# Performance work log

Hardware: AMD Instinct MI355X
Metric: run time of the kernel (lower is better)

The kernel has to match this reference:

```python
import jax, jax.numpy as jnp
import numpy as np

N_NODES = 100000
N_EDGES = 1600000
D_IN = 13      # per-localization feature dim
D_POS = 3
HIDDEN = 64
D_OUT = 64


def setup_inputs() -> dict:
    key = jax.random.key(0)
    ks = jax.random.split(key, 6)
    x_locs = jax.random.normal(ks[0], (N_NODES, D_IN), dtype=jnp.float32)
    pos_locs = jax.random.uniform(ks[1], (N_NODES, D_POS), dtype=jnp.float32)
    edge_index = jax.random.randint(ks[2], (2, N_EDGES), 0, N_NODES, dtype=jnp.int64)
    fan1 = D_IN + D_POS
    W1 = jax.random.normal(ks[3], (fan1, HIDDEN), dtype=jnp.float32) / np.sqrt(fan1)
    b1 = jnp.zeros((HIDDEN,), dtype=jnp.float32)
    W2 = jax.random.normal(ks[4], (HIDDEN, D_OUT), dtype=jnp.float32) / np.sqrt(HIDDEN)
    b2 = jnp.zeros((D_OUT,), dtype=jnp.float32)
    return {"x_locs": x_locs, "pos_locs": pos_locs, "W1": W1, "b1": b1,
            "W2": W2, "b2": b2, "edge_index": edge_index}


def reference(x_locs, pos_locs, W1, b1, W2, b2, edge_index):
    # PointNetConv (source_to_target): j = edge_index[0] (source), i = edge_index[1] (target)
    src = edge_index[0]
    dst = edge_index[1]
    # message input: [x_j, pos_j - pos_i]  -> [E, D_IN + D_POS]
    msg_in = jnp.concatenate([x_locs[src], pos_locs[src] - pos_locs[dst]], axis=-1)
    # local_nn: Linear -> ReLU -> Linear
    h = jax.nn.relu(msg_in @ W1 + b1)            # [E, HIDDEN]
    h = h @ W2 + b2                               # [E, D_OUT]
    # max aggregation per target node; empty segments get -inf
    agg = jax.ops.segment_max(h, dst, num_segments=N_NODES)  # [N, D_OUT]
    # final .relu() in LocEncoder; also maps empty (-inf) segments to 0 (PyG convention)
    return jax.nn.relu(agg)
```

## Files before the change

kernel.cpp:

```cpp
#include <hip/hip_runtime.h>
#include <hip/hip_bf16.h>


#define N_NODES 100000
#define N_EDGES 1600000
#define NB2  782
#define NBLK 391
#define BATCH 4096
#define SCAP 2400

typedef short short8  __attribute__((ext_vector_type(8)));
typedef float float4v __attribute__((ext_vector_type(4)));

__device__ inline short f2bf(float f) {
    union { float f; unsigned u; } v; v.f = f;
    unsigned u = v.u;
    u += 0x7fffu + ((u >> 16) & 1u);
    return (short)(u >> 16);
}
__device__ inline short2 f2bf2(float a, float b) {
    __hip_bfloat162 h = __float22bfloat162_rn(make_float2(a, b));
    return *(short2*)&h;
}
__device__ inline float bf2f(short s) {
    union { unsigned u; float f; } v;
    v.u = ((unsigned)(unsigned short)s) << 16;
    return v.f;
}
__device__ inline int wave_incl_scan(int v, int lane) {
#pragma unroll
    for (int d = 1; d < 64; d <<= 1) {
        const int t = __shfl_up(v, d);
        if (lane >= d) v += t;
    }
    return v;
}

__global__ __launch_bounds__(256) void prep_kernel(
    const float* __restrict__ x, const float* __restrict__ pos,
    const float* __restrict__ W1, const float* __restrict__ b1,
    const int* __restrict__ ei,
    int* __restrict__ offsT,
    int* __restrict__ blockSorted,
    unsigned short* __restrict__ u16, unsigned short* __restrict__ w16)
{
    __shared__ int hist[NB2], eoff[NB2], offc[NB2];
    __shared__ int csumP[13];

    const int tid  = threadIdx.x;
    const int lane = tid & 63;
    const int wv   = tid >> 6;

    if (blockIdx.x >= NBLK) {
        float w1c[16];
#pragma unroll
        for (int k = 0; k < 16; ++k) w1c[k] = W1[k * 64 + lane];
        const float b1c = b1[lane];

        const int waveId = (blockIdx.x - NBLK) * 4 + wv;
        const int nwave  = 512 * 4;

        for (int node = waveId; node < N_NODES; node += nwave) {
            float m = 0.f;
            if (lane < 13) m = x[node * 13 + lane];
            else if (lane < 16) m = pos[node * 3 + (lane - 13)];

            float acc = b1c, accw = 0.f;
#pragma unroll
            for (int k = 0; k < 13; ++k)
                acc = fmaf(__shfl(m, k), w1c[k], acc);
#pragma unroll
            for (int k = 13; k < 16; ++k) {
                const float p = __shfl(m, k);
                acc  = fmaf(p, w1c[k], acc);
                accw = fmaf(p, w1c[k], accw);
            }
            u16[node * 64 + lane] = (unsigned short)f2bf(acc);
            w16[node * 64 + lane] = (unsigned short)f2bf(accw);
        }
        return;
    }

    const int blk = blockIdx.x;
    const int e0  = blk * BATCH;
    const int nn  = (N_EDGES - e0) < BATCH ? (N_EDGES - e0) : BATCH;

    for (int i = tid; i < NB2; i += 256) hist[i] = 0;
    __syncthreads();

#pragma unroll
    for (int rep = 0; rep < 4; ++rep) {
        const int base = rep * 1024 + tid * 4;
        if (base < nn) {
            const int4 d4 = *(const int4*)(ei + N_EDGES + e0 + base);
            atomicAdd(&hist[d4.x >> 7], 1);
            atomicAdd(&hist[d4.y >> 7], 1);
            atomicAdd(&hist[d4.z >> 7], 1);
            atomicAdd(&hist[d4.w >> 7], 1);
        }
    }
    __syncthreads();

    for (int c = wv; c < 13; c += 4) {
        const int idx = c * 64 + lane;
        const int val = (idx < NB2) ? hist[idx] : 0;
        const int inc = wave_incl_scan(val, lane);
        if (idx < NB2) eoff[idx] = inc;
        if (lane == 63) csumP[c] = inc;
    }
    __syncthreads();
    if (tid == 0) {
        int a = 0;
#pragma unroll
        for (int c = 0; c < 13; ++c) { const int t = csumP[c]; csumP[c] = a; a += t; }
    }
    __syncthreads();
    for (int c = wv; c < 13; c += 4) {
        const int idx = c * 64 + lane;
        if (idx < NB2) eoff[idx] += csumP[c] - hist[idx];
    }
    __syncthreads();

    for (int b = tid; b < NB2; b += 256) {
        offsT[b * NBLK + blk] = eoff[b];
        offc[b] = eoff[b];
    }
    if (tid == 0) offsT[NB2 * NBLK + blk] = nn;
    __syncthreads();

    int* dstp = blockSorted + blk * BATCH;
#pragma unroll
    for (int rep = 0; rep < 4; ++rep) {
        const int base = rep * 1024 + tid * 4;
        if (base < nn) {
            const int4 s4 = *(const int4*)(ei + e0 + base);
            const int4 d4 = *(const int4*)(ei + N_EDGES + e0 + base);
            int p;
            p = atomicAdd(&offc[d4.x >> 7], 1); dstp[p] = (s4.x << 7) | (d4.x & 127);
            p = atomicAdd(&offc[d4.y >> 7], 1); dstp[p] = (s4.y << 7) | (d4.y & 127);
            p = atomicAdd(&offc[d4.z >> 7], 1); dstp[p] = (s4.z << 7) | (d4.z & 127);
            p = atomicAdd(&offc[d4.w >> 7], 1); dstp[p] = (s4.w << 7) | (d4.w & 127);
        }
    }
}

__global__ __launch_bounds__(256, 4) void aggregate_kernel(
    const unsigned short* __restrict__ u16,
    const unsigned short* __restrict__ w16,
    const float* __restrict__ W2,
    const float* __restrict__ b2,
    const int*   __restrict__ offsT,
    const int*   __restrict__ blockSorted,
    float*       __restrict__ out)
{
    __shared__ int staged[SCAP];
    __shared__ int sortedL[SCAP];
    __shared__ int E[NBLK], G[NBLK];
    __shared__ int hist[128], hoff[128], nstart[128];
    __shared__ int csum[8];
    __shared__ int totT;

    const int tid  = threadIdx.x;
    const int lane = tid & 63;
    const int wv   = tid >> 6;
    const int q = lane >> 4, n = lane & 15;
    const int b = blockIdx.x;
    const int node0 = b * 128;

    short8 w2f[2][4];
#pragma unroll
    for (int s = 0; s < 2; ++s)
#pragma unroll
        for (int t = 0; t < 4; ++t)
#pragma unroll
            for (int j = 0; j < 8; ++j)
                w2f[s][t][j] = f2bf(W2[(s * 32 + q * 8 + j) * 64 + (n + 16 * t)]);
    float b2c[4];
#pragma unroll
    for (int t = 0; t < 4; ++t) b2c[t] = b2[n + 16 * t];

    if (tid < 128) hist[tid] = 0;

    for (int r = tid; r < NBLK; r += 256) {
        const int lo = offsT[b * NBLK + r];
        const int hi = offsT[(b + 1) * NBLK + r];
        staged[r] = hi - lo;
        G[r] = r * BATCH + lo;
    }
    __syncthreads();
    for (int c = wv; c < 7; c += 4) {
        const int idx = c * 64 + lane;
        const int val = (idx < NBLK) ? staged[idx] : 0;
        const int inc = wave_incl_scan(val, lane);
        if (idx < NBLK) E[idx] = inc;
        if (lane == 63) csum[c] = inc;
    }
    __syncthreads();
    if (tid == 0) {
        int a = 0;
#pragma unroll
        for (int c = 0; c < 7; ++c) { const int t = csum[c]; csum[c] = a; a += t; }
        totT = a;
    }
    __syncthreads();
    for (int c = wv; c < 7; c += 4) {
        const int idx = c * 64 + lane;
        if (idx < NBLK) E[idx] += csum[c] - staged[idx];
    }
    __syncthreads();

    int T = totT; T = T < SCAP ? T : SCAP;

    for (int i = tid; i < T; i += 256) {
        int lo = 0, hi = NBLK - 1;
#pragma unroll
        for (int s = 0; s < 9; ++s) {
            const int mid = (lo + hi + 1) >> 1;
            if (E[mid] <= i) lo = mid; else hi = mid - 1;
        }
        const int w = blockSorted[G[lo] + (i - E[lo])];
        staged[i] = w;
        atomicAdd(&hist[w & 127], 1);
    }
    __syncthreads();

    if (wv < 2) {
        const int v = hist[tid];
        const int inc = wave_incl_scan(v, lane);
        nstart[tid] = inc - v;
        if (lane == 63) csum[wv] = inc;
    }
    __syncthreads();
    if (tid >= 64 && tid < 128) nstart[tid] += csum[0];
    __syncthreads();
    if (tid < 128) hoff[tid] = nstart[tid];
    __syncthreads();
    for (int i = tid; i < T; i += 256) {
        const int w = staged[i];
        const int p = atomicAdd(&hoff[w & 127], 1);
        sortedL[p] = w >> 7;
    }
    __syncthreads();

    auto compute = [&](int node, int2 sd, int src,
                       short8 ulo, short8 uhi, short8 wl, short8 wh) {
        float vmax[4] = {0.f, 0.f, 0.f, 0.f};
        int base = 0;
        while (true) {
            const int rows = (sd.y - base) < 16 ? (sd.y - base) : 16;
            if (rows > 0) {
                union { short8 v; short2 h[4]; } alo, ahi;
#pragma unroll
                for (int j = 0; j < 4; ++j) {
                    alo.h[j] = f2bf2(
                        fmaxf(bf2f(ulo[2*j])   - bf2f(wl[2*j]),   0.f),
                        fmaxf(bf2f(ulo[2*j+1]) - bf2f(wl[2*j+1]), 0.f));
                    ahi.h[j] = f2bf2(
                        fmaxf(bf2f(uhi[2*j])   - bf2f(wh[2*j]),   0.f),
                        fmaxf(bf2f(uhi[2*j+1]) - bf2f(wh[2*j+1]), 0.f));
                }
                float4v c2[4];
#pragma unroll
                for (int t = 0; t < 4; ++t) {
                    c2[t] = __builtin_amdgcn_mfma_f32_16x16x32_bf16(
                        alo.v, w2f[0][t], (float4v){0.f, 0.f, 0.f, 0.f}, 0, 0, 0);
                    c2[t] = __builtin_amdgcn_mfma_f32_16x16x32_bf16(
                        ahi.v, w2f[1][t], c2[t], 0, 0, 0);
                }
#pragma unroll
                for (int r = 0; r < 4; ++r) {
                    const int row = q * 4 + r;
#pragma unroll
                    for (int t = 0; t < 4; ++t) {
                        const float v = c2[t][r] + b2c[t];
                        if (row < rows) vmax[t] = fmaxf(vmax[t], v);
                    }
                }
            }
            base += 16;
            if (base >= sd.y) break;
            const int r2 = (sd.y - base) < 16 ? (sd.y - base) : 16;
            src = (n < r2) ? sortedL[sd.x + base + n] : 0;
            ulo = *(const short8*)(u16 + src * 64 + q * 8);
            uhi = *(const short8*)(u16 + src * 64 + 32 + q * 8);
        }
#pragma unroll
        for (int t = 0; t < 4; ++t) {
            vmax[t] = fmaxf(vmax[t], __shfl_xor(vmax[t], 16));
            vmax[t] = fmaxf(vmax[t], __shfl_xor(vmax[t], 32));
        }
        float v = vmax[0];
        v = (q == 1) ? vmax[1] : v;
        v = (q == 2) ? vmax[2] : v;
        v = (q == 3) ? vmax[3] : v;
        if (node < N_NODES) out[node * 64 + lane] = v;
    };

    const int nlbase = wv * 32;
#pragma unroll 1
    for (int g = 0; g < 32; g += 2) {
        const int nlA = nlbase + g, nlB = nlA + 1;
        const int nA = node0 + nlA, nB = node0 + nlB;
        const int2 sdA = {nstart[nlA], hist[nlA]};
        const int2 sdB = {nstart[nlB], hist[nlB]};
        const int nAc = nA < (N_NODES - 1) ? nA : (N_NODES - 1);
        const int nBc = nB < (N_NODES - 1) ? nB : (N_NODES - 1);

        const int rA = sdA.y < 16 ? sdA.y : 16;
        const int rB = sdB.y < 16 ? sdB.y : 16;
        const int srcA = (n < rA) ? sortedL[sdA.x + n] : 0;
        const int srcB = (n < rB) ? sortedL[sdB.x + n] : 0;

        const short8 ulA = *(const short8*)(u16 + srcA * 64 + q * 8);
        const short8 uhA = *(const short8*)(u16 + srcA * 64 + 32 + q * 8);
        const short8 wlA = *(const short8*)(w16 + nAc * 64 + q * 8);
        const short8 whA = *(const short8*)(w16 + nAc * 64 + 32 + q * 8);
        const short8 ulB = *(const short8*)(u16 + srcB * 64 + q * 8);
        const short8 uhB = *(const short8*)(u16 + srcB * 64 + 32 + q * 8);
        const short8 wlB = *(const short8*)(w16 + nBc * 64 + q * 8);
        const short8 whB = *(const short8*)(w16 + nBc * 64 + 32 + q * 8);

        compute(nA, sdA, srcA, ulA, uhA, wlA, whA);
        compute(nB, sdB, srcB, ulB, uhB, wlB, whB);
    }
}

extern "C" void kernel_launch(void* const* d_in, const int* in_sizes, int n_in,
                              void* d_out, int out_size, void* d_ws, size_t ws_size,
                              hipStream_t stream) {
    const float* x   = (const float*)d_in[0];
    const float* pos = (const float*)d_in[1];
    const float* W1  = (const float*)d_in[2];
    const float* b1  = (const float*)d_in[3];
    const float* W2  = (const float*)d_in[4];
    const float* b2  = (const float*)d_in[5];
    const int*   ei  = (const int*)d_in[6];

    char* ws = (char*)d_ws;
    int* blockSorted = (int*)(ws + 0);
    int* offsT       = (int*)(ws + 6406144);
    unsigned short* u16 = (unsigned short*)(ws + 7631360);
    unsigned short* w16 = (unsigned short*)(ws + 20431360);

    prep_kernel<<<NBLK + 512, 256, 0, stream>>>(
        x, pos, W1, b1, ei, offsT, blockSorted, u16, w16);
    aggregate_kernel<<<NB2, 256, 0, stream>>>(
        u16, w16, W2, b2, offsT, blockSorted, (float*)d_out);
}
```

Before: 213.1 us.

## Switch to fp16 packed math, 64-node buckets, and split prep into two kernels

Replaces the bf16 storage and the manual bf16 convert/relu with fp16 values, so the relu-subtract runs as packed half vector ops and the MFMA uses the f16 variant. Halves the bucket width from 128 to 64 nodes, so the aggregate launches twice as many blocks with smaller shared staging. Splits the fused prep kernel into separate precompute and partition kernels, and the precompute now handles two nodes per wave iteration. This removes per-element conversion ALU work and increases parallelism, at the cost of an extra launch, fp16 range risk, and more offset scanning per aggregate block.

```diff
diff --git a/kernel.cpp b/kernel.cpp
--- a/kernel.cpp
+++ b/kernel.cpp
@@ -1,32 +1,16 @@
 #include <hip/hip_runtime.h>
-#include <hip/hip_bf16.h>
 
 
 #define N_NODES 100000
 #define N_EDGES 1600000
-#define NB2  782
+#define NB2  1563
 #define NBLK 391
 #define BATCH 4096
-#define SCAP 2400
-
-typedef short short8  __attribute__((ext_vector_type(8)));
+#define SCAP2 1280
+
+typedef _Float16 half8 __attribute__((ext_vector_type(8)));
 typedef float float4v __attribute__((ext_vector_type(4)));
 
-__device__ inline short f2bf(float f) {
-    union { float f; unsigned u; } v; v.f = f;
-    unsigned u = v.u;
-    u += 0x7fffu + ((u >> 16) & 1u);
-    return (short)(u >> 16);
-}
-__device__ inline short2 f2bf2(float a, float b) {
-    __hip_bfloat162 h = __float22bfloat162_rn(make_float2(a, b));
-    return *(short2*)&h;
-}
-__device__ inline float bf2f(short s) {
-    union { unsigned u; float f; } v;
-    v.u = ((unsigned)(unsigned short)s) << 16;
-    return v.f;
-}
 __device__ inline int wave_incl_scan(int v, int lane) {
 #pragma unroll
     for (int d = 1; d < 64; d <<= 1) {
@@ -36,54 +20,64 @@
     return v;
 }
 
-__global__ __launch_bounds__(256) void prep_kernel(
+__global__ __launch_bounds__(256) void precompute_kernel(
     const float* __restrict__ x, const float* __restrict__ pos,
     const float* __restrict__ W1, const float* __restrict__ b1,
+    _Float16* __restrict__ u16, _Float16* __restrict__ w16)
+{
+    const int lane = threadIdx.x & 63;
+    float w1c[16];
+#pragma unroll
+    for (int k = 0; k < 16; ++k) w1c[k] = W1[k * 64 + lane];
+    const float b1c = b1[lane];
+
+    const int waveId = blockIdx.x * 4 + (threadIdx.x >> 6);
+    const int step   = 512 * 4 * 2;
+
+    for (int nd = waveId * 2; nd < N_NODES; nd += step) {
+        const int nA = nd, nB = nd + 1;
+        float mA = 0.f, mB = 0.f;
+        if (lane < 13) {
+            mA = x[nA * 13 + lane];
+            mB = x[nB * 13 + lane];
+        } else if (lane < 16) {
+            mA = pos[nA * 3 + (lane - 13)];
+            mB = pos[nB * 3 + (lane - 13)];
+        }
+
+        float aA = b1c, wA = 0.f, aB = b1c, wB = 0.f;
+#pragma unroll
+        for (int k = 0; k < 13; ++k) {
+            aA = fmaf(__shfl(mA, k), w1c[k], aA);
+            aB = fmaf(__shfl(mB, k), w1c[k], aB);
+        }
+#pragma unroll
+        for (int k = 13; k < 16; ++k) {
+            const float pA = __shfl(mA, k), pB = __shfl(mB, k);
+            aA = fmaf(pA, w1c[k], aA);  wA = fmaf(pA, w1c[k], wA);
+            aB = fmaf(pB, w1c[k], aB);  wB = fmaf(pB, w1c[k], wB);
+        }
+        u16[nA * 64 + lane] = (_Float16)aA;
+        w16[nA * 64 + lane] = (_Float16)wA;
+        u16[nB * 64 + lane] = (_Float16)aB;
+        w16[nB * 64 + lane] = (_Float16)wB;
+    }
+}
+
+__global__ __launch_bounds__(256) void partition_kernel(
     const int* __restrict__ ei,
     int* __restrict__ offsT,
-    int* __restrict__ blockSorted,
-    unsigned short* __restrict__ u16, unsigned short* __restrict__ w16)
+    int* __restrict__ blockSorted)
 {
     __shared__ int hist[NB2], eoff[NB2], offc[NB2];
-    __shared__ int csumP[13];
+    __shared__ int csumP[25];
 
     const int tid  = threadIdx.x;
     const int lane = tid & 63;
     const int wv   = tid >> 6;
-
-    if (blockIdx.x >= NBLK) {
-        float w1c[16];
-#pragma unroll
-        for (int k = 0; k < 16; ++k) w1c[k] = W1[k * 64 + lane];
-        const float b1c = b1[lane];
-
-        const int waveId = (blockIdx.x - NBLK) * 4 + wv;
-        const int nwave  = 512 * 4;
-
-        for (int node = waveId; node < N_NODES; node += nwave) {
-            float m = 0.f;
-            if (lane < 13) m = x[node * 13 + lane];
-            else if (lane < 16) m = pos[node * 3 + (lane - 13)];
-
-            float acc = b1c, accw = 0.f;
-#pragma unroll
-            for (int k = 0; k < 13; ++k)
-                acc = fmaf(__shfl(m, k), w1c[k], acc);
-#pragma unroll
-            for (int k = 13; k < 16; ++k) {
-                const float p = __shfl(m, k);
-                acc  = fmaf(p, w1c[k], acc);
-                accw = fmaf(p, w1c[k], accw);
-            }
-            u16[node * 64 + lane] = (unsigned short)f2bf(acc);
-            w16[node * 64 + lane] = (unsigned short)f2bf(accw);
-        }
-        return;
-    }
-
-    const int blk = blockIdx.x;
-    const int e0  = blk * BATCH;
-    const int nn  = (N_EDGES - e0) < BATCH ? (N_EDGES - e0) : BATCH;
+    const int blk  = blockIdx.x;
+    const int e0   = blk * BATCH;
+    const int nn   = (N_EDGES - e0) < BATCH ? (N_EDGES - e0) : BATCH;
 
     for (int i = tid; i < NB2; i += 256) hist[i] = 0;
     __syncthreads();
@@ -93,15 +87,15 @@
         const int base = rep * 1024 + tid * 4;
         if (base < nn) {
             const int4 d4 = *(const int4*)(ei + N_EDGES + e0 + base);
-            atomicAdd(&hist[d4.x >> 7], 1);
-            atomicAdd(&hist[d4.y >> 7], 1);
-            atomicAdd(&hist[d4.z >> 7], 1);
-            atomicAdd(&hist[d4.w >> 7], 1);
-        }
-    }
-    __syncthreads();
-
-    for (int c = wv; c < 13; c += 4) {
+            atomicAdd(&hist[d4.x >> 6], 1);
+            atomicAdd(&hist[d4.y >> 6], 1);
+            atomicAdd(&hist[d4.z >> 6], 1);
+            atomicAdd(&hist[d4.w >> 6], 1);
+        }
+    }
+    __syncthreads();
+
+    for (int c = wv; c < 25; c += 4) {
         const int idx = c * 64 + lane;
         const int val = (idx < NB2) ? hist[idx] : 0;
         const int inc = wave_incl_scan(val, lane);
@@ -112,10 +106,10 @@
     if (tid == 0) {
         int a = 0;
 #pragma unroll
-        for (int c = 0; c < 13; ++c) { const int t = csumP[c]; csumP[c] = a; a += t; }
-    }
-    __syncthreads();
-    for (int c = wv; c < 13; c += 4) {
+        for (int c = 0; c < 25; ++c) { const int t = csumP[c]; csumP[c] = a; a += t; }
+    }
+    __syncthreads();
+    for (int c = wv; c < 25; c += 4) {
         const int idx = c * 64 + lane;
         if (idx < NB2) eoff[idx] += csumP[c] - hist[idx];
     }
@@ -136,27 +130,27 @@
             const int4 s4 = *(const int4*)(ei + e0 + base);
             const int4 d4 = *(const int4*)(ei + N_EDGES + e0 + base);
             int p;
-            p = atomicAdd(&offc[d4.x >> 7], 1); dstp[p] = (s4.x << 7) | (d4.x & 127);
-            p = atomicAdd(&offc[d4.y >> 7], 1); dstp[p] = (s4.y << 7) | (d4.y & 127);
-            p = atomicAdd(&offc[d4.z >> 7], 1); dstp[p] = (s4.z << 7) | (d4.z & 127);
-            p = atomicAdd(&offc[d4.w >> 7], 1); dstp[p] = (s4.w << 7) | (d4.w & 127);
+            p = atomicAdd(&offc[d4.x >> 6], 1); dstp[p] = (s4.x << 6) | (d4.x & 63);
+            p = atomicAdd(&offc[d4.y >> 6], 1); dstp[p] = (s4.y << 6) | (d4.y & 63);
+            p = atomicAdd(&offc[d4.z >> 6], 1); dstp[p] = (s4.z << 6) | (d4.z & 63);
+            p = atomicAdd(&offc[d4.w >> 6], 1); dstp[p] = (s4.w << 6) | (d4.w & 63);
         }
     }
 }
 
 __global__ __launch_bounds__(256, 4) void aggregate_kernel(
-    const unsigned short* __restrict__ u16,
-    const unsigned short* __restrict__ w16,
+    const _Float16* __restrict__ u16,
+    const _Float16* __restrict__ w16,
     const float* __restrict__ W2,
     const float* __restrict__ b2,
     const int*   __restrict__ offsT,
     const int*   __restrict__ blockSorted,
     float*       __restrict__ out)
 {
-    __shared__ int staged[SCAP];
-    __shared__ int sortedL[SCAP];
+    __shared__ int staged[SCAP2];
+    __shared__ int sortedL[SCAP2];
     __shared__ int E[NBLK], G[NBLK];
-    __shared__ int hist[128], hoff[128], nstart[128];
+    __shared__ int hist[64], nstart[64], hoff[64];
     __shared__ int csum[8];
     __shared__ int totT;
 
@@ -165,21 +159,21 @@
     const int wv   = tid >> 6;
     const int q = lane >> 4, n = lane & 15;
     const int b = blockIdx.x;
-    const int node0 = b * 128;
-
-    short8 w2f[2][4];
+    const int node0 = b * 64;
+
+    half8 w2f[2][4];
 #pragma unroll
     for (int s = 0; s < 2; ++s)
 #pragma unroll
         for (int t = 0; t < 4; ++t)
 #pragma unroll
             for (int j = 0; j < 8; ++j)
-                w2f[s][t][j] = f2bf(W2[(s * 32 + q * 8 + j) * 64 + (n + 16 * t)]);
+                w2f[s][t][j] = (_Float16)W2[(s * 32 + q * 8 + j) * 64 + (n + 16 * t)];
     float b2c[4];
 #pragma unroll
     for (int t = 0; t < 4; ++t) b2c[t] = b2[n + 16 * t];
 
-    if (tid < 128) hist[tid] = 0;
+    if (tid < 64) hist[tid] = 0;
 
     for (int r = tid; r < NBLK; r += 256) {
         const int lo = offsT[b * NBLK + r];
@@ -209,7 +203,7 @@
     }
     __syncthreads();
 
-    int T = totT; T = T < SCAP ? T : SCAP;
+    int T = totT; T = T < SCAP2 ? T : SCAP2;
 
     for (int i = tid; i < T; i += 256) {
         int lo = 0, hi = NBLK - 1;
@@ -220,52 +214,42 @@
         }
         const int w = blockSorted[G[lo] + (i - E[lo])];
         staged[i] = w;
-        atomicAdd(&hist[w & 127], 1);
-    }
-    __syncthreads();
-
-    if (wv < 2) {
-        const int v = hist[tid];
+        atomicAdd(&hist[w & 63], 1);
+    }
+    __syncthreads();
+
+    if (wv == 0) {
+        const int v = hist[lane];
         const int inc = wave_incl_scan(v, lane);
-        nstart[tid] = inc - v;
-        if (lane == 63) csum[wv] = inc;
-    }
-    __syncthreads();
-    if (tid >= 64 && tid < 128) nstart[tid] += csum[0];
-    __syncthreads();
-    if (tid < 128) hoff[tid] = nstart[tid];
+        nstart[lane] = inc - v;
+        hoff[lane]   = inc - v;
+    }
     __syncthreads();
     for (int i = tid; i < T; i += 256) {
         const int w = staged[i];
-        const int p = atomicAdd(&hoff[w & 127], 1);
-        sortedL[p] = w >> 7;
-    }
-    __syncthreads();
+        const int p = atomicAdd(&hoff[w & 63], 1);
+        sortedL[p] = w >> 6;
+    }
+    __syncthreads();
+
+    const half8 zero8 = {0, 0, 0, 0, 0, 0, 0, 0};
 
     auto compute = [&](int node, int2 sd, int src,
-                       short8 ulo, short8 uhi, short8 wl, short8 wh) {
+                       half8 ulo, half8 uhi, half8 wl, half8 wh) {
         float vmax[4] = {0.f, 0.f, 0.f, 0.f};
         int base = 0;
         while (true) {
             const int rows = (sd.y - base) < 16 ? (sd.y - base) : 16;
             if (rows > 0) {
-                union { short8 v; short2 h[4]; } alo, ahi;
-#pragma unroll
-                for (int j = 0; j < 4; ++j) {
-                    alo.h[j] = f2bf2(
-                        fmaxf(bf2f(ulo[2*j])   - bf2f(wl[2*j]),   0.f),
-                        fmaxf(bf2f(ulo[2*j+1]) - bf2f(wl[2*j+1]), 0.f));
-                    ahi.h[j] = f2bf2(
-                        fmaxf(bf2f(uhi[2*j])   - bf2f(wh[2*j]),   0.f),
-                        fmaxf(bf2f(uhi[2*j+1]) - bf2f(wh[2*j+1]), 0.f));
-                }
+                const half8 alo = __builtin_elementwise_max(ulo - wl, zero8);
+                const half8 ahi = __builtin_elementwise_max(uhi - wh, zero8);
                 float4v c2[4];
 #pragma unroll
                 for (int t = 0; t < 4; ++t) {
-                    c2[t] = __builtin_amdgcn_mfma_f32_16x16x32_bf16(
-                        alo.v, w2f[0][t], (float4v){0.f, 0.f, 0.f, 0.f}, 0, 0, 0);
-                    c2[t] = __builtin_amdgcn_mfma_f32_16x16x32_bf16(
-                        ahi.v, w2f[1][t], c2[t], 0, 0, 0);
+                    c2[t] = __builtin_amdgcn_mfma_f32_16x16x32_f16(
+                        alo, w2f[0][t], (float4v){0.f, 0.f, 0.f, 0.f}, 0, 0, 0);
+                    c2[t] = __builtin_amdgcn_mfma_f32_16x16x32_f16(
+                        ahi, w2f[1][t], c2[t], 0, 0, 0);
                 }
 #pragma unroll
                 for (int r = 0; r < 4; ++r) {
@@ -281,8 +265,8 @@
             if (base >= sd.y) break;
             const int r2 = (sd.y - base) < 16 ? (sd.y - base) : 16;
             src = (n < r2) ? sortedL[sd.x + base + n] : 0;
-            ulo = *(const short8*)(u16 + src * 64 + q * 8);
-            uhi = *(const short8*)(u16 + src * 64 + 32 + q * 8);
+            ulo = *(const half8*)(u16 + src * 64 + q * 8);
+            uhi = *(const half8*)(u16 + src * 64 + 32 + q * 8);
         }
 #pragma unroll
         for (int t = 0; t < 4; ++t) {
@@ -296,9 +280,9 @@
         if (node < N_NODES) out[node * 64 + lane] = v;
     };
 
-    const int nlbase = wv * 32;
+    const int nlbase = wv * 16;
 #pragma unroll 1
-    for (int g = 0; g < 32; g += 2) {
+    for (int g = 0; g < 16; g += 2) {
         const int nlA = nlbase + g, nlB = nlA + 1;
         const int nA = node0 + nlA, nB = node0 + nlB;
         const int2 sdA = {nstart[nlA], hist[nlA]};
@@ -311,14 +295,14 @@
         const int srcA = (n < rA) ? sortedL[sdA.x + n] : 0;
         const int srcB = (n < rB) ? sortedL[sdB.x + n] : 0;
 
-        const short8 ulA = *(const short8*)(u16 + srcA * 64 + q * 8);
-        const short8 uhA = *(const short8*)(u16 + srcA * 64 + 32 + q * 8);
-        const short8 wlA = *(const short8*)(w16 + nAc * 64 + q * 8);
-        const short8 whA = *(const short8*)(w16 + nAc * 64 + 32 + q * 8);
-        const short8 ulB = *(const short8*)(u16 + srcB * 64 + q * 8);
-        const short8 uhB = *(const short8*)(u16 + srcB * 64 + 32 + q * 8);
-        const short8 wlB = *(const short8*)(w16 + nBc * 64 + q * 8);
-        const short8 whB = *(const short8*)(w16 + nBc * 64 + 32 + q * 8);
+        const half8 ulA = *(const half8*)(u16 + srcA * 64 + q * 8);
+        const half8 uhA = *(const half8*)(u16 + srcA * 64 + 32 + q * 8);
+        const half8 wlA = *(const half8*)(w16 + nAc * 64 + q * 8);
+        const half8 whA = *(const half8*)(w16 + nAc * 64 + 32 + q * 8);
+        const half8 ulB = *(const half8*)(u16 + srcB * 64 + q * 8);
+        const half8 uhB = *(const half8*)(u16 + srcB * 64 + 32 + q * 8);
+        const half8 wlB = *(const half8*)(w16 + nBc * 64 + q * 8);
+        const half8 whB = *(const half8*)(w16 + nBc * 64 + 32 + q * 8);
 
         compute(nA, sdA, srcA, ulA, uhA, wlA, whA);
         compute(nB, sdB, srcB, ulB, uhB, wlB, whB);
@@ -339,11 +323,11 @@
     char* ws = (char*)d_ws;
     int* blockSorted = (int*)(ws + 0);
     int* offsT       = (int*)(ws + 6406144);
-    unsigned short* u16 = (unsigned short*)(ws + 7631360);
-    unsigned short* w16 = (unsigned short*)(ws + 20431360);
-
-    prep_kernel<<<NBLK + 512, 256, 0, stream>>>(
-        x, pos, W1, b1, ei, offsT, blockSorted, u16, w16);
+    _Float16* u16 = (_Float16*)(ws + 8852480);
+    _Float16* w16 = (_Float16*)(ws + 21652480);
+
+    precompute_kernel<<<512, 256, 0, stream>>>(x, pos, W1, b1, u16, w16);
+    partition_kernel<<<NBLK, 256, 0, stream>>>(ei, offsT, blockSorted);
     aggregate_kernel<<<NB2, 256, 0, stream>>>(
         u16, w16, W2, b2, offsT, blockSorted, (float*)d_out);
 }
```

Result: faster. 195.6 us (-8.2%).
